# Performance work log

Hardware: AMD Instinct MI355X
Metric: run time of the kernel (lower is better)

## Reference

```python
import jax, jax.numpy as jnp
import numpy as np


def _lstm_layer(x, W_ih, W_hh, b_ih, b_hh):
    # x: [B, T, D_in]; W_ih: [4H, D_in]; W_hh: [4H, H]; gate order i,f,g,o (PyTorch).
    B, T, _ = x.shape
    H = W_hh.shape[1]
    # Precompute all input projections once (batched GEMM over time).
    x_proj = jnp.einsum('bti,gi->btg', x, W_ih) + b_ih + b_hh  # [B, T, 4H]
    x_proj = jnp.transpose(x_proj, (1, 0, 2))                  # [T, B, 4H]

    def step(carry, xt):
        h, c = carry
        gates = xt + h @ W_hh.T                                # [B, 4H]
        i, f, g, o = jnp.split(gates, 4, axis=-1)
        i = jax.nn.sigmoid(i)
        f = jax.nn.sigmoid(f)
        g = jnp.tanh(g)
        o = jax.nn.sigmoid(o)
        c = f * c + i * g
        h = o * jnp.tanh(c)
        return (h, c), h

    h0 = jnp.zeros((B, H), dtype=x.dtype)
    c0 = jnp.zeros((B, H), dtype=x.dtype)
    (_, _), hs = jax.lax.scan(step, (h0, c0), x_proj)          # hs: [T, B, H]
    return jnp.transpose(hs, (1, 0, 2))                        # [B, T, H]


def setup_inputs() -> dict:
    key = jax.random.key(0)
    ks = jax.random.split(key, 12)
    B, T, D, H, O = 4096, 512, 5, 50, 1
    s = 1.0 / np.sqrt(H)  # torch default init scale
    u = lambda k, shape: jax.random.uniform(k, shape, jnp.float32, -s, s)
    return {
        'x': jax.random.normal(ks[0], (B, T, D), jnp.float32),
        'W_ih0': u(ks[1], (4 * H, D)),
        'W_hh0': u(ks[2], (4 * H, H)),
        'b_ih0': u(ks[3], (4 * H,)),
        'b_hh0': u(ks[4], (4 * H,)),
        'W_ih1': u(ks[5], (4 * H, H)),
        'W_hh1': u(ks[6], (4 * H, H)),
        'b_ih1': u(ks[7], (4 * H,)),
        'b_hh1': u(ks[8], (4 * H,)),
        'W_lin': u(ks[9], (O, H)),
        'b_lin': u(ks[10], (O,)),
    }


def reference(x, W_ih0, W_hh0, b_ih0, b_hh0, W_ih1, W_hh1, b_ih1, b_hh1, W_lin, b_lin):
    # 2-layer LSTM (eval mode: inter-layer dropout inactive) + linear head on last step.
    h1 = _lstm_layer(x, W_ih0, W_hh0, b_ih0, b_hh0)   # [B, T, H]
    h2 = _lstm_layer(h1, W_ih1, W_hh1, b_ih1, b_hh1)  # [B, T, H]
    last = h2[:, -1, :]                               # [B, H]
    return last @ W_lin.T + b_lin                     # [B, 1]
```

## Files before the change

kernel.cpp:

```cpp
#include <hip/hip_runtime.h>


#define NB 16
#define BLK 512
#define TT 512
#define LOG2E 1.44269504088896340736f
#define SA 72
#define SXR 264

typedef _Float16 half8 __attribute__((ext_vector_type(8)));
typedef __attribute__((ext_vector_type(4))) float f32x4;

#define MFMAH(a, b, c) __builtin_amdgcn_mfma_f32_16x16x32_f16((a), (b), (c), 0, 0, 0)

__device__ __forceinline__ float fexp2(float x) { return __builtin_amdgcn_exp2f(x); }
__device__ __forceinline__ float frcp(float x)  { return __builtin_amdgcn_rcpf(x); }

#define CELL_UPDATE(ACCX, BUF, WBX)                                         \
    _Pragma("unroll")                                                       \
    for (int r = 0; r < 4; ++r) {                                           \
        float eu = fexp2(ACCX[0][r]);                                \
        float ew = fexp2(ACCX[1][r]);                                \
        float ev = fexp2(ACCX[2][r]);                     \
        float ey = fexp2(ACCX[3][r]);                                \
        float pu = 1.f + eu, pw = 1.f + ew, pv = 1.f + ev;                  \
        float P  = pu * pv;                                                 \
        float rD = frcp(P * pw);                                            \
        float N  = cst[r] * P + (2.f - pv) * pw;                            \
        float cn = N * rD;                                                  \
        cst[r] = cn;                                                        \
        float za = fminf(cn * (-2.f * LOG2E), 80.f);                        \
        float ez = fexp2(za);                                               \
        float pz = 1.f + ez, py = 1.f + ey;                                 \
        float rQ = frcp(py * pz);                                           \
        float h  = (2.f - pz) * rQ;                                         \
        if (jv) BUF[WBX][(4 * c + r) * SA + j] = (_Float16)h;               \
    }

#define TICK(T, RB, WB)                                                     \
    {                                                                       \
        if (grp == 0) {                                                     \
            if ((T) < TT) {                                                 \
                __builtin_amdgcn_s_setprio(1);                              \
                half8 a0 = *(const half8*)&sA0[RB][ln * SA + 0 + 8 * c];    \
                half8 a1 = *(const half8*)&sA0[RB][ln * SA + 32 + 8 * c];   \
                             \
                if ((T) < TT - 1 && xlane) {                                \
                    int tl1 = ((T) + 1) & 31;                               \
                    sA0[WB][xb * SA + 50 + xd] =                            \
                        (_Float16)sX[xb * SXR + tl1 * 8 + xd];              \
                }                                                           \
                f32x4 acc[4];                                               \
                _Pragma("unroll")                                           \
                for (int p = 0; p < 4; ++p) {                               \
                    acc[p] = MFMAH(a0, bfr[p][0], bias4[p]);                \
                    acc[p] = MFMAH(a1, bfr[p][1], acc[p]);                  \
                }                                                           \
                __builtin_amdgcn_s_setprio(0);                              \
                CELL_UPDATE(acc, sA0, WB)                                   \
            }                                                               \
        } else {                                                            \
            if ((T) > 0) {                                                  \
                __builtin_amdgcn_s_setprio(1);                              \
                half8 a0 = *(const half8*)&sA0[RB][ln * SA + 0 + 8 * c];    \
                half8 a1 = *(const half8*)&sA0[RB][ln * SA + 32 + 8 * c];   \
                half8 a2 = *(const half8*)&sA1[RB][ln * SA + 0 + 8 * c];    \
                half8 a3 = *(const half8*)&sA1[RB][ln * SA + 32 + 8 * c];   \
                f32x4 acc[4];                                               \
                _Pragma("unroll")                                           \
                for (int p = 0; p < 4; ++p) {                               \
                    acc[p] = MFMAH(a0, bfr[p][0], bias4[p]);                \
                    acc[p] = MFMAH(a1, bfr[p][1], acc[p]);                  \
                    acc[p] = MFMAH(a2, bfr[p][2], acc[p]);                  \
                    acc[p] = MFMAH(a3, bfr[p][3], acc[p]);                  \
                }                                                           \
                __builtin_amdgcn_s_setprio(0);                              \
                CELL_UPDATE(acc, sA1, WB)                                   \
            }                                                               \
        }                                                                   \
        __syncthreads();                                                    \
    }

#define STAGE(T)                                                            \
    if ((T) < TT - 1) {                                                     \
        _Pragma("unroll")                                                   \
        for (int q = 0; q < 5; ++q) {                                       \
            int e = tid + q * BLK, b_ = e / 160, r_ = e - b_ * 160;         \
            int ts = r_ / 5, d_ = r_ - ts * 5;                              \
            sX[b_ * SXR + ts * 8 + d_] = xr[q];                             \
        }                                                                   \
        if ((T) + 33 < TT) {                                                \
            _Pragma("unroll")                                               \
            for (int q = 0; q < 5; ++q) {                                   \
                int e = tid + q * BLK, b_ = e / 160, r_ = e - b_ * 160;     \
                xr[q] = x[(size_t)(bb0 + b_) * 2560 +                       \
                          (size_t)((T) + 33) * 5 + r_];                     \
            }                                                               \
        }                                                                   \
        __syncthreads();                                                    \
    }

__global__ __launch_bounds__(512, 2) void lstm2_v7(
    const float* __restrict__ x,
    const float* __restrict__ Wih0,
    const float* __restrict__ Whh0,
    const float* __restrict__ bih0,
    const float* __restrict__ bhh0,
    const float* __restrict__ Wih1,
    const float* __restrict__ Whh1,
    const float* __restrict__ bih1,
    const float* __restrict__ bhh1,
    const float* __restrict__ Wlin,
    const float* __restrict__ blin,
    float* __restrict__ out)
{
    __shared__ __align__(16) _Float16 sA0[2][16 * SA];
    __shared__ __align__(16) _Float16 sA1[2][16 * SA];
    __shared__ __align__(16) float sX[16 * SXR];

    const int tid = threadIdx.x;
    const int w = tid >> 6, l = tid & 63, c = l >> 4, ln = l & 15;
    const int grp = w >> 2, wl = w & 3;
    const int bb0 = blockIdx.x * NB;
    const int j = 16 * wl + ln;
    const bool jv = (j < 50);

    const bool xlane = (grp == 0) && (l < 20);
    const int xb = 4 * w + l / 5, xd = l % 5;

    for (int i = tid; i < 2 * 16 * SA; i += BLK) {
        (&sA0[0][0])[i] = (_Float16)0.f;
        (&sA1[0][0])[i] = (_Float16)0.f;
    }

    half8 bfr[4][4];
    f32x4 bias4[4];
#pragma unroll
    for (int p = 0; p < 4; ++p) {
        const float gs = (p == 2) ? (-2.f * LOG2E) : (-LOG2E);
        const int g = p * 50 + j;
#pragma unroll
        for (int s = 0; s < 4; ++s) {
            half8 tb;
#pragma unroll
            for (int jj = 0; jj < 8; ++jj) {
                int k = 32 * s + 8 * c + jj;
                float v = 0.f;
                if (jv) {
                    if (grp == 0) {
                        if (k < 50)      v = Whh0[g * 50 + k];
                        else if (k < 55) v = Wih0[g * 5 + (k - 50)];
                    } else {
                        if (k < 50)                  v = Wih1[g * 50 + k];
                        else if (k >= 64 && k < 114) v = Whh1[g * 50 + (k - 64)];
                    }
                }
                tb[jj] = (_Float16)(v * gs);
            }
            bfr[p][s] = tb;
        }
        float bv = jv ? ((grp == 0) ? (bih0[g] + bhh0[g]) : (bih1[g] + bhh1[g])) : 0.f;
        bv *= gs;
        f32x4 b4; b4[0] = bv; b4[1] = bv; b4[2] = bv; b4[3] = bv;
        bias4[p] = b4;
    }

    float cst[4] = {0.f, 0.f, 0.f, 0.f};

    float xr[5];
#pragma unroll
    for (int q = 0; q < 5; ++q) {
        int e = tid + q * BLK, b = e / 160, r = e - b * 160;
        xr[q] = x[(size_t)(bb0 + b) * 2560 + r];
    }
#pragma unroll
    for (int q = 0; q < 5; ++q) {
        int e = tid + q * BLK, b = e / 160, r = e - b * 160;
        int ts = r / 5, d = r - ts * 5;
        sX[b * SXR + ts * 8 + d] = xr[q];
    }
#pragma unroll
    for (int q = 0; q < 5; ++q) {
        int e = tid + q * BLK, b = e / 160, r = e - b * 160;
        xr[q] = x[(size_t)(bb0 + b) * 2560 + 160 + r];
    }
    __syncthreads();

    if (tid < 80) {
        int b = tid / 5, d = tid - 5 * b;
        sA0[1][b * SA + 50 + d] = (_Float16)x[(size_t)(bb0 + b) * 2560 + d];
    }
    __syncthreads();

    for (int t = 0; t < TT; t += 2) {
        TICK(t, 1, 0)
        if ((t & 31) == 30) { STAGE(t + 1) }
        TICK(t + 1, 0, 1)
    }
    TICK(TT, 1, 0)

    if (tid < NB) {
        float s = blin[0];
#pragma unroll
        for (int jj = 0; jj < 50; ++jj)
            s += Wlin[jj] * (float)sA1[0][tid * SA + jj];
        out[bb0 + tid] = s;
    }
}

extern "C" void kernel_launch(void* const* d_in, const int* in_sizes, int n_in,
                              void* d_out, int out_size, void* d_ws, size_t ws_size,
                              hipStream_t stream) {
    (void)in_sizes; (void)n_in; (void)d_ws; (void)ws_size; (void)out_size;
    const float* x    = (const float*)d_in[0];
    const float* Wih0 = (const float*)d_in[1];
    const float* Whh0 = (const float*)d_in[2];
    const float* bih0 = (const float*)d_in[3];
    const float* bhh0 = (const float*)d_in[4];
    const float* Wih1 = (const float*)d_in[5];
    const float* Whh1 = (const float*)d_in[6];
    const float* bih1 = (const float*)d_in[7];
    const float* bhh1 = (const float*)d_in[8];
    const float* Wlin = (const float*)d_in[9];
    const float* blin = (const float*)d_in[10];

    lstm2_v7<<<dim3(256), dim3(512), 0, stream>>>(
        x, Wih0, Whh0, bih0, bhh0, Wih1, Whh1, bih1, bhh1, Wlin, blin,
        (float*)d_out);
}
```

Measured before the change: 374.8 us.

## Skew layer-1 by an extra step with triple-buffered layer-0 hidden state

Layer-0 hidden states move to a three-slot rotating buffer, and layer 1 now lags layer 0 by two steps instead of one. Layer 1 loads its input-projection operand (h0) into registers one tick ahead and starts the MFMAs on those registers before it reads its own recurrent state from LDS. The aim is to hide the LDS read latency on the layer-1 critical path. In exchange the loop runs one extra tick, adds rotating buffer indices and per-thread register state, and uses more shared memory.

```diff
diff --git a/kernel.cpp b/kernel.cpp
--- a/kernel.cpp
+++ b/kernel.cpp
@@ -16,7 +16,7 @@
 __device__ __forceinline__ float fexp2(float x) { return __builtin_amdgcn_exp2f(x); }
 __device__ __forceinline__ float frcp(float x)  { return __builtin_amdgcn_rcpf(x); }
 
-#define CELL_UPDATE(ACCX, BUF, WBX)                                         \
+#define CELL_UPDATE(ACCX, DST, GUARD)                                       \
     _Pragma("unroll")                                                       \
     for (int r = 0; r < 4; ++r) {                                           \
         float eu = fexp2(ACCX[0][r]);                                \
@@ -34,20 +34,20 @@
         float pz = 1.f + ez, py = 1.f + ey;                                 \
         float rQ = frcp(py * pz);                                           \
         float h  = (2.f - pz) * rQ;                                         \
-        if (jv) BUF[WBX][(4 * c + r) * SA + j] = (_Float16)h;               \
-    }
-
-#define TICK(T, RB, WB)                                                     \
+        if (GUARD) (DST)[(4 * c + r) * SA + j] = (_Float16)h;               \
+    }
+
+#define TICK(T, RB1, WB1)                                                   \
     {                                                                       \
         if (grp == 0) {                                                     \
             if ((T) < TT) {                                                 \
                 __builtin_amdgcn_s_setprio(1);                              \
-                half8 a0 = *(const half8*)&sA0[RB][ln * SA + 0 + 8 * c];    \
-                half8 a1 = *(const half8*)&sA0[RB][ln * SA + 32 + 8 * c];   \
+                half8 a0 = *(const half8*)&sA0[r3][ln * SA + 0 + 8 * c];    \
+                half8 a1 = *(const half8*)&sA0[r3][ln * SA + 32 + 8 * c];   \
                              \
                 if ((T) < TT - 1 && xlane) {                                \
                     int tl1 = ((T) + 1) & 31;                               \
-                    sA0[WB][xb * SA + 50 + xd] =                            \
+                    sA0[w3][xb * SA + 50 + xd] =                            \
                         (_Float16)sX[xb * SXR + tl1 * 8 + xd];              \
                 }                                                           \
                 f32x4 acc[4];                                               \
@@ -57,28 +57,38 @@
                     acc[p] = MFMAH(a1, bfr[p][1], acc[p]);                  \
                 }                                                           \
                 __builtin_amdgcn_s_setprio(0);                              \
-                CELL_UPDATE(acc, sA0, WB)                                   \
+                CELL_UPDATE(acc, &sA0[w3][0], jv)                           \
             }                                                               \
         } else {                                                            \
-            if ((T) > 0) {                                                  \
+            if ((T) >= 2) {                                                 \
                 __builtin_amdgcn_s_setprio(1);                              \
-                half8 a0 = *(const half8*)&sA0[RB][ln * SA + 0 + 8 * c];    \
-                half8 a1 = *(const half8*)&sA0[RB][ln * SA + 32 + 8 * c];   \
-                half8 a2 = *(const half8*)&sA1[RB][ln * SA + 0 + 8 * c];    \
-                half8 a3 = *(const half8*)&sA1[RB][ln * SA + 32 + 8 * c];   \
+                half8 a2 = *(const half8*)&sA1[RB1][ln * SA + 0 + 8 * c];   \
+                half8 a3 = *(const half8*)&sA1[RB1][ln * SA + 32 + 8 * c];  \
                 f32x4 acc[4];                                               \
                 _Pragma("unroll")                                           \
+                for (int p = 0; p < 4; ++p)                                 \
+                    acc[p] = MFMAH(l1a0, bfr[p][0], bias4[p]);              \
+                _Pragma("unroll")                                           \
+                for (int p = 0; p < 4; ++p)                                 \
+                    acc[p] = MFMAH(l1a1, bfr[p][1], acc[p]);                \
+                \
+                \
+                l1a0 = *(const half8*)&sA0[r3][ln * SA + 0 + 8 * c];        \
+                l1a1 = *(const half8*)&sA0[r3][ln * SA + 32 + 8 * c];       \
+                _Pragma("unroll")                                           \
                 for (int p = 0; p < 4; ++p) {                               \
-                    acc[p] = MFMAH(a0, bfr[p][0], bias4[p]);                \
-                    acc[p] = MFMAH(a1, bfr[p][1], acc[p]);                  \
                     acc[p] = MFMAH(a2, bfr[p][2], acc[p]);                  \
                     acc[p] = MFMAH(a3, bfr[p][3], acc[p]);                  \
                 }                                                           \
                 __builtin_amdgcn_s_setprio(0);                              \
-                CELL_UPDATE(acc, sA1, WB)                                   \
+                CELL_UPDATE(acc, &sA1[WB1][0], true)                        \
+            } else if ((T) == 1) {                                          \
+                l1a0 = *(const half8*)&sA0[r3][ln * SA + 0 + 8 * c];        \
+                l1a1 = *(const half8*)&sA0[r3][ln * SA + 32 + 8 * c];       \
             }                                                               \
         }                                                                   \
         __syncthreads();                                                    \
+        r3 = w3; w3 = (w3 == 2) ? 0 : (w3 + 1);                             \
     }
 
 #define STAGE(T)                                                            \
@@ -100,7 +110,7 @@
         __syncthreads();                                                    \
     }
 
-__global__ __launch_bounds__(512, 2) void lstm2_v7(
+__global__ __launch_bounds__(512, 2) void lstm2_v8(
     const float* __restrict__ x,
     const float* __restrict__ Wih0,
     const float* __restrict__ Whh0,
@@ -114,7 +124,7 @@
     const float* __restrict__ blin,
     float* __restrict__ out)
 {
-    __shared__ __align__(16) _Float16 sA0[2][16 * SA];
+    __shared__ __align__(16) _Float16 sA0[3][16 * SA];
     __shared__ __align__(16) _Float16 sA1[2][16 * SA];
     __shared__ __align__(16) float sX[16 * SXR];
 
@@ -128,10 +138,8 @@
     const bool xlane = (grp == 0) && (l < 20);
     const int xb = 4 * w + l / 5, xd = l % 5;
 
-    for (int i = tid; i < 2 * 16 * SA; i += BLK) {
-        (&sA0[0][0])[i] = (_Float16)0.f;
-        (&sA1[0][0])[i] = (_Float16)0.f;
-    }
+    for (int i = tid; i < 3 * 16 * SA; i += BLK) (&sA0[0][0])[i] = (_Float16)0.f;
+    for (int i = tid; i < 2 * 16 * SA; i += BLK) (&sA1[0][0])[i] = (_Float16)0.f;
 
     half8 bfr[4][4];
     f32x4 bias4[4];
@@ -166,6 +174,8 @@
     }
 
     float cst[4] = {0.f, 0.f, 0.f, 0.f};
+    half8 l1a0 = {}, l1a1 = {};
+    int r3 = 2, w3 = 0;
 
     float xr[5];
 #pragma unroll
@@ -188,22 +198,21 @@
 
     if (tid < 80) {
         int b = tid / 5, d = tid - 5 * b;
-        sA0[1][b * SA + 50 + d] = (_Float16)x[(size_t)(bb0 + b) * 2560 + d];
+        sA0[2][b * SA + 50 + d] = (_Float16)x[(size_t)(bb0 + b) * 2560 + d];
     }
     __syncthreads();
 
-    for (int t = 0; t < TT; t += 2) {
+    for (int t = 0; t < TT + 2; t += 2) {
         TICK(t, 1, 0)
         if ((t & 31) == 30) { STAGE(t + 1) }
         TICK(t + 1, 0, 1)
     }
-    TICK(TT, 1, 0)
 
     if (tid < NB) {
         float s = blin[0];
 #pragma unroll
         for (int jj = 0; jj < 50; ++jj)
-            s += Wlin[jj] * (float)sA1[0][tid * SA + jj];
+            s += Wlin[jj] * (float)sA1[1][tid * SA + jj];
         out[bb0 + tid] = s;
     }
 }
@@ -224,7 +233,7 @@
     const float* Wlin = (const float*)d_in[9];
     const float* blin = (const float*)d_in[10];
 
-    lstm2_v7<<<dim3(256), dim3(512), 0, stream>>>(
+    lstm2_v8<<<dim3(256), dim3(512), 0, stream>>>(
         x, Wih0, Whh0, bih0, bhh0, Wih1, Whh1, bih1, bhh1, Wlin, blin,
         (float*)d_out);
 }
```

Result: faster. 352.0 us (-6.1%).
